# Performance work log

Hardware: AMD Instinct MI355X
Metric: run time of the kernel (lower is better)

The kernel has to match this reference:

```python
import jax, jax.numpy as jnp
import numpy as np

B, S, D, E = 8, 2048, 4096, 64
EXPERT_CAPACITY = 40  # seq_len / n_experts * 1.25


def setup_inputs() -> dict:
    key = jax.random.key(0)
    k1, k2 = jax.random.split(key)
    hidden_states = jax.random.normal(k1, (B, S, D), dtype=jnp.float32)
    W = jax.random.normal(k2, (D, E), dtype=jnp.float32) * (1.0 / np.sqrt(D))
    b = jnp.zeros((E,), dtype=jnp.float32)
    return {"hidden_states": hidden_states, "W": W, "b": b}


def reference(hidden_states, W, b):
    # router logits: [B, S, E] (jitter_noise == 0, router_dtype == float32)
    router_logits = jnp.einsum('bsd,de->bse', hidden_states, W) + b
    router_probs = jax.nn.softmax(router_logits, axis=-1)
    top1_probs = jnp.max(router_probs, axis=-1)                    # [B, S]
    expert_idx = jnp.argmax(router_probs, axis=-1)                 # [B, S]
    expert_indices = jax.nn.one_hot(expert_idx, E, dtype=jnp.int32)  # [B, S, E]
    # capacity masking: cumulative token priority per expert along seq dim
    token_priority = jnp.cumsum(expert_indices, axis=-2)           # [B, S, E]
    capacity_mask = token_priority <= EXPERT_CAPACITY
    expert_indices = expert_indices * capacity_mask.astype(jnp.int32)
    num_dropped = jnp.sum(jnp.sum(expert_indices, axis=-1) == 0)
    # aux load-balancing loss
    fi = jnp.sum(expert_indices, axis=-2).astype(router_probs.dtype) / S  # [B, E]
    pi = jnp.sum(router_probs, axis=-2) / S                               # [B, E]
    aux_loss = jnp.mean(E * jnp.sum(fi * pi, axis=-1))
    return (expert_indices, top1_probs, router_probs, aux_loss, num_dropped)
```

## Files before the change

### kernel.cpp

```cpp
#include <hip/hip_runtime.h>
#include <hip/hip_bf16.h>
#include <stdint.h>

#define Bb 8
#define Ss 2048
#define Dd 4096
#define Ee 64
#define CAP 40
#define M_TOK (Bb*Ss)
#define TOP1_OFF  (M_TOK*Ee)
#define PROBS_OFF (TOP1_OFF + M_TOK)
#define AUX_OFF   (PROBS_OFF + M_TOK*Ee)
#define ND_OFF    (AUX_OFF + 1)

#define W2_OFF   0u
#define PART_OFF (1u<<20)
#define CNTT_OFF (17u<<20)
#define PIT_OFF  ((17u<<20) + (64u<<10))
#define EID_OFF  ((17u<<20) + (128u<<10))

typedef __attribute__((ext_vector_type(8))) short short8;
typedef __attribute__((ext_vector_type(4))) float f32x4;

#define FENCE() do {                                                          \
    asm volatile("" ::: "memory");                                            \
    __builtin_amdgcn_sched_barrier(0);                                        \
  } while (0)

__device__ __forceinline__ void cvt8hl(const float4 a, const float4 b,
                                       short8& hi, short8& lo) {
  __hip_bfloat162 h0 = __float22bfloat162_rn(make_float2(a.x, a.y));
  __hip_bfloat162 h1 = __float22bfloat162_rn(make_float2(a.z, a.w));
  __hip_bfloat162 h2 = __float22bfloat162_rn(make_float2(b.x, b.y));
  __hip_bfloat162 h3 = __float22bfloat162_rn(make_float2(b.z, b.w));
  float2 f0 = __bfloat1622float2(h0), f1 = __bfloat1622float2(h1);
  float2 f2 = __bfloat1622float2(h2), f3 = __bfloat1622float2(h3);
  __hip_bfloat162 l0 = __float22bfloat162_rn(make_float2(a.x - f0.x, a.y - f0.y));
  __hip_bfloat162 l1 = __float22bfloat162_rn(make_float2(a.z - f1.x, a.w - f1.y));
  __hip_bfloat162 l2 = __float22bfloat162_rn(make_float2(b.x - f2.x, b.y - f2.y));
  __hip_bfloat162 l3 = __float22bfloat162_rn(make_float2(b.z - f3.x, b.w - f3.y));
  union U { __hip_bfloat162 h[4]; short8 s; };
  U uh; uh.h[0] = h0; uh.h[1] = h1; uh.h[2] = h2; uh.h[3] = h3; hi = uh.s;
  U ul; ul.h[0] = l0; ul.h[1] = l1; ul.h[2] = l2; ul.h[3] = l3; lo = ul.s;
}

__global__ __launch_bounds__(256) void k0_wsplit(const float* __restrict__ W,
                                                 char* __restrict__ w2) {
  const int id  = blockIdx.x * 256 + threadIdx.x;
  const int l   = id & 63;
  const int g   = (id >> 6) & 3;
  const int sub = (id >> 8) & 1;
  const int c   = id >> 9;
  const int e   = g * 16 + (l & 15);
  const int kb  = c * 64 + sub * 32 + (l >> 4) * 8;
  float xs[8];
#pragma unroll
  for (int j = 0; j < 8; ++j) xs[j] = W[(size_t)(kb + j) * Ee + e];
  short8 hi, lo;
  cvt8hl(make_float4(xs[0], xs[1], xs[2], xs[3]),
         make_float4(xs[4], xs[5], xs[6], xs[7]), hi, lo);
  char* base = w2 + (size_t)c * 16384 + sub * 8192 + g * 2048 + l * 16;
  *(short8*)base = hi;
  *(short8*)(base + 1024) = lo;
}

__global__ __launch_bounds__(256, 4) void k1_gemm(
    const float* __restrict__ H, const char* __restrict__ w2,
    float* __restrict__ part) {
  __shared__ char wb[4][8192];
  const int tid = threadIdx.x;
  const int wv = tid >> 6, l = tid & 63;
  const int tg = blockIdx.x >> 2, ks = blockIdx.x & 3;
  const float* hA = H + (size_t)(tg * 64 + wv * 16 + (l & 15)) * Dd
                      + ks * 1024 + (l >> 4) * 8;
  const char* wsrc = w2 + (size_t)ks * 262144 + wv * 2048 + l * 16;

  f32x4 acc[4];
#pragma unroll
  for (int g = 0; g < 4; ++g) acc[g] = (f32x4){0.f, 0.f, 0.f, 0.f};

  float4 aX0, aX1, aY0, aY1;
  short8 ah0, al0;

#define GLL16(gs, ls)                                                         \
  __builtin_amdgcn_global_load_lds(                                           \
      (const __attribute__((address_space(1))) unsigned int*)(gs),            \
      (__attribute__((address_space(3))) unsigned int*)(ls), 16, 0, 0)

#define STAGE(t, bi) {                                                        \
    const char* s_ = wsrc + (size_t)(t) * 8192;                               \
    char* d_ = &wb[bi][wv * 2048];                                            \
    GLL16(s_, d_); GLL16(s_ + 1024, d_ + 1024); }

#define LDA(r0, r1, t) { const float* p_ = hA + (t) * 32;                     \
    r0 = *(const float4*)(p_); r1 = *(const float4*)(p_ + 4); }

#define MFMA4(ac, ah, al, wh, wl) {                                           \
    ac = __builtin_amdgcn_mfma_f32_16x16x32_bf16(ah, wh, ac, 0, 0, 0);        \
    ac = __builtin_amdgcn_mfma_f32_16x16x32_bf16(ah, wl, ac, 0, 0, 0);        \
    ac = __builtin_amdgcn_mfma_f32_16x16x32_bf16(al, wh, ac, 0, 0, 0);        \
    ac = __builtin_amdgcn_mfma_f32_16x16x32_bf16(al, wl, ac, 0, 0, 0); }

#define COMPM(bi) { const char* wp_ = &wb[bi][0] + l * 16;                    \
    _Pragma("unroll")                                                         \
    for (int g = 0; g < 4; ++g) {                                             \
      const short8 wh = *(const short8*)(wp_ + g * 2048);                     \
      const short8 wl = *(const short8*)(wp_ + g * 2048 + 1024);              \
      MFMA4(acc[g], ah0, al0, wh, wl);                                        \
    } }

  STAGE(0, 0);
  FENCE();
  asm volatile("s_waitcnt vmcnt(0)" ::: "memory");
  __builtin_amdgcn_s_barrier();
  STAGE(1, 1);
  FENCE();
  LDA(aX0, aX1, 0);
  FENCE();
  STAGE(2, 2);
  FENCE();
  LDA(aY0, aY1, 1);
  FENCE();

#pragma unroll
  for (int t = 0; t < 32; ++t) {
    if (t < 30)       { asm volatile("s_waitcnt vmcnt(4)" ::: "memory"); }
    else if (t == 30) { asm volatile("s_waitcnt vmcnt(2)" ::: "memory"); }
    else              { asm volatile("s_waitcnt vmcnt(0)" ::: "memory"); }
    FENCE();
    if ((t & 1) == 0) { cvt8hl(aX0, aX1, ah0, al0); }
    else              { cvt8hl(aY0, aY1, ah0, al0); }
    FENCE();
    if (t <= 28) STAGE(t + 3, (t + 3) & 3);
    FENCE();
    if (t <= 29) {
      if ((t & 1) == 0) { LDA(aX0, aX1, t + 2); }
      else              { LDA(aY0, aY1, t + 2); }
    }
    FENCE();
    COMPM(t & 3);
    if (t < 31) __builtin_amdgcn_s_barrier();
  }

  float* pp = part + (size_t)(tg * 4 + ks) * 4096;
#pragma unroll
  for (int g = 0; g < 4; ++g)
#pragma unroll
    for (int r = 0; r < 4; ++r)
      pp[(wv * 16 + (l >> 4) * 4 + r) * 64 + g * 16 + (l & 15)] = acc[g][r];
}

__global__ __launch_bounds__(512) void k1b_softmax(
    const float* __restrict__ part, const float* __restrict__ bias,
    float* __restrict__ out, int* __restrict__ cntT, float* __restrict__ piT,
    int* __restrict__ eid_ws) {
  __shared__ int   csh[512];
  __shared__ float psh[512];
  const int tid = threadIdx.x, wv = tid >> 6, l = tid & 63;
  const int tg = blockIdx.x;
  const float* p0 = part + (size_t)tg * 16384;

  int cnt = 0; float pis = 0.f;
  const float bl_ = bias[l];
#pragma unroll
  for (int i = 0; i < 8; ++i) {
    const int t = wv * 8 + i, tok = tg * 64 + t;
    const float v = p0[t * 64 + l] + p0[4096 + t * 64 + l] +
                    p0[8192 + t * 64 + l] + p0[12288 + t * 64 + l] + bl_;
    float m = v; int mi = l;
#pragma unroll
    for (int off = 32; off >= 1; off >>= 1) {
      const float ov = __shfl_xor(m, off);
      const int   oi = __shfl_xor(mi, off);
      if (ov > m || (ov == m && oi < mi)) { m = ov; mi = oi; }
    }
    const float ex = __expf(v - m);
    float ssum = ex;
#pragma unroll
    for (int off = 32; off >= 1; off >>= 1) ssum += __shfl_xor(ssum, off);
    const float inv = 1.0f / ssum;
    const float p = ex * inv;
    out[(size_t)PROBS_OFF + (size_t)tok * Ee + l] = p;
    if (l == 0) {
      out[TOP1_OFF + tok] = inv;
      eid_ws[tok] = mi;
    }
    cnt += (mi == l) ? 1 : 0;
    pis += p;
  }
  csh[wv * 64 + l] = cnt;
  psh[wv * 64 + l] = pis;
  __syncthreads();
  if (tid < 64) {
    int ct = 0; float pp = 0.f;
#pragma unroll
    for (int w = 0; w < 8; ++w) { ct += csh[w * 64 + tid]; pp += psh[w * 64 + tid]; }
    cntT[((size_t)(tg >> 5) * 64 + tid) * 32 + (tg & 31)] = ct;
    piT [((size_t)(tg >> 5) * 64 + tid) * 32 + (tg & 31)] = pp;
  }
}

__global__ __launch_bounds__(64) void k3_indices(
    const int* __restrict__ cntT, const float* __restrict__ piT,
    const int* __restrict__ eid_ws, float* __restrict__ out) {
  __shared__ float tile[64][64];
  const int g = blockIdx.x, lane = threadIdx.x;
  const int b = g >> 5, cc = g & 31;
  const int tok = g * 64 + lane;
  const int e = eid_ws[tok];

  unsigned long long mymask = 0ull;
  for (int j = 0; j < 64; ++j) {
    const int ej = __shfl(e, j);
    const unsigned long long bal = __ballot(ej == e);
    if (j == lane) mymask = bal;
  }
  const int lrank = __popcll(mymask & ((1ull << lane) - 1ull));

  const int4* cp = (const int4*)(cntT + ((size_t)b * 64 + e) * 32);
  int prefix = 0;
#pragma unroll
  for (int j = 0; j < 8; ++j) {
    const int4 v = cp[j];
    const int base = 4 * j;
    prefix += ((base + 0 < cc) ? v.x : 0) + ((base + 1 < cc) ? v.y : 0)
            + ((base + 2 < cc) ? v.z : 0) + ((base + 3 < cc) ? v.w : 0);
  }
  const float keep = (prefix + lrank < CAP) ? 1.0f : 0.0f;

#pragma unroll
  for (int j = 0; j < 64; ++j) tile[j][lane] = 0.f;
  __syncthreads();
  tile[lane][e] = keep;
  __syncthreads();

  float4*       og = (float4*)(out + (size_t)g * 64 * 64);
  const float4* ts = (const float4*)&tile[0][0];
#pragma unroll
  for (int i = 0; i < 16; ++i) og[i * 64 + lane] = ts[i * 64 + lane];

  if (g == 0) {
    float auxsum = 0.f; int dropped = 0;
    for (int bb = 0; bb < 8; ++bb) {
      const int4*   cq = (const int4*)  (cntT + ((size_t)bb * 64 + lane) * 32);
      const float4* pq = (const float4*)(piT  + ((size_t)bb * 64 + lane) * 32);
      int tot = 0; float ps = 0.f;
#pragma unroll
      for (int j = 0; j < 8; ++j) {
        const int4 v = cq[j];   tot += v.x + v.y + v.z + v.w;
        const float4 w = pq[j]; ps  += w.x + w.y + w.z + w.w;
      }
      dropped += (tot > CAP) ? (tot - CAP) : 0;
      const float fi = (float)((tot < CAP) ? tot : CAP) * (1.0f / (float)Ss);
      const float pi = ps * (1.0f / (float)Ss);
      float fp = fi * pi;
#pragma unroll
      for (int off = 32; off >= 1; off >>= 1) fp += __shfl_xor(fp, off);
      auxsum += fp;
    }
#pragma unroll
    for (int off = 32; off >= 1; off >>= 1) dropped += __shfl_xor(dropped, off);
    if (lane == 0) {
      out[AUX_OFF] = (float)Ee * auxsum / (float)Bb;
      out[ND_OFF]  = (float)dropped;
    }
  }
}

extern "C" void kernel_launch(void* const* d_in, const int* in_sizes, int n_in,
                              void* d_out, int out_size, void* d_ws, size_t ws_size,
                              hipStream_t stream) {
  const float* H    = (const float*)d_in[0];
  const float* Wm   = (const float*)d_in[1];
  const float* bias = (const float*)d_in[2];
  float* out = (float*)d_out;
  char*  w2   = (char*) d_ws + W2_OFF;
  float* part = (float*)((char*)d_ws + PART_OFF);
  int*   cntT = (int*)  ((char*)d_ws + CNTT_OFF);
  float* piT  = (float*)((char*)d_ws + PIT_OFF);
  int*   eid  = (int*)  ((char*)d_ws + EID_OFF);

  hipLaunchKernelGGL(k0_wsplit,   dim3(128),  dim3(256), 0, stream, Wm, w2);
  hipLaunchKernelGGL(k1_gemm,     dim3(1024), dim3(256), 0, stream, H, w2, part);
  hipLaunchKernelGGL(k1b_softmax, dim3(256),  dim3(512), 0, stream,
                     part, bias, out, cntT, piT, eid);
  hipLaunchKernelGGL(k3_indices,  dim3(256),  dim3(64),  0, stream,
                     cntT, piT, eid, out);
}
```

Baseline: 90.24 us.

## Stage activation tiles through LDS via async global_load_lds with XOR swizzle

The GEMM kernel now loads the fp32 hidden-state tiles asynchronously into LDS with global_load_lds, alongside the weights, instead of holding them in register double-buffers. The LDS tiles use an XOR swizzle to avoid bank conflicts, and the bf16 hi/lo split now happens after reading from LDS. The barrier moves to the top of each iteration and the vmcnt thresholds are adjusted to match. LDS per block doubles and the launch-bounds occupancy hint drops from 4 to 2, so fewer blocks may be resident, in exchange for lower register pressure and fully asynchronous A loads.

```diff
diff --git a/kernel.cpp b/kernel.cpp
--- a/kernel.cpp
+++ b/kernel.cpp
@@ -64,22 +64,23 @@
   *(short8*)(base + 1024) = lo;
 }
 
-__global__ __launch_bounds__(256, 4) void k1_gemm(
+__global__ __launch_bounds__(256, 2) void k1_gemm(
     const float* __restrict__ H, const char* __restrict__ w2,
     float* __restrict__ part) {
-  __shared__ char wb[4][8192];
+  __shared__ char wb[4][16384];
   const int tid = threadIdx.x;
   const int wv = tid >> 6, l = tid & 63;
   const int tg = blockIdx.x >> 2, ks = blockIdx.x & 3;
-  const float* hA = H + (size_t)(tg * 64 + wv * 16 + (l & 15)) * Dd
-                      + ks * 1024 + (l >> 4) * 8;
+  const int tb = tg * 64;
   const char* wsrc = w2 + (size_t)ks * 262144 + wv * 2048 + l * 16;
+  const int swz = ((l & 7) ^ (l >> 3)) * 4;
+  const float* asrc0 = H + (size_t)(tb + wv * 8 + (l >> 3)) * Dd
+                         + ks * 1024 + swz;
+  const float* asrc1 = asrc0 + (size_t)32 * Dd;
 
   f32x4 acc[4];
 #pragma unroll
   for (int g = 0; g < 4; ++g) acc[g] = (f32x4){0.f, 0.f, 0.f, 0.f};
-
-  float4 aX0, aX1, aY0, aY1;
   short8 ah0, al0;
 
 #define GLL16(gs, ls)                                                         \
@@ -88,12 +89,14 @@
       (__attribute__((address_space(3))) unsigned int*)(ls), 16, 0, 0)
 
 #define STAGE(t, bi) {                                                        \
-    const char* s_ = wsrc + (size_t)(t) * 8192;                               \
-    char* d_ = &wb[bi][wv * 2048];                                            \
-    GLL16(s_, d_); GLL16(s_ + 1024, d_ + 1024); }
-
-#define LDA(r0, r1, t) { const float* p_ = hA + (t) * 32;                     \
-    r0 = *(const float4*)(p_); r1 = *(const float4*)(p_ + 4); }
+    const char* sw_ = wsrc + (size_t)(t) * 8192;                              \
+    char* dw_ = &wb[bi][wv * 2048];                                           \
+    GLL16(sw_, dw_); GLL16(sw_ + 1024, dw_ + 1024);                           \
+    const float* sa0_ = asrc0 + (t) * 32;                                     \
+    const float* sa1_ = asrc1 + (t) * 32;                                     \
+    char* da0_ = &wb[bi][8192 + wv * 1024];                                   \
+    char* da1_ = &wb[bi][8192 + 4096 + wv * 1024];                            \
+    GLL16(sa0_, da0_); GLL16(sa1_, da1_); }
 
 #define MFMA4(ac, ah, al, wh, wl) {                                           \
     ac = __builtin_amdgcn_mfma_f32_16x16x32_bf16(ah, wh, ac, 0, 0, 0);        \
@@ -101,7 +104,16 @@
     ac = __builtin_amdgcn_mfma_f32_16x16x32_bf16(al, wh, ac, 0, 0, 0);        \
     ac = __builtin_amdgcn_mfma_f32_16x16x32_bf16(al, wl, ac, 0, 0, 0); }
 
-#define COMPM(bi) { const char* wp_ = &wb[bi][0] + l * 16;                    \
+  const int arow = wv * 16 + (l & 15);
+  const int aslot0 = ((2 * (l >> 4))     ^ (arow & 7)) * 16;
+  const int aslot1 = ((2 * (l >> 4) + 1) ^ (arow & 7)) * 16;
+
+#define COMPM(bi) {                                                           \
+    const char* ab_ = &wb[bi][8192] + arow * 128;                             \
+    const float4 fa_ = *(const float4*)(ab_ + aslot0);                        \
+    const float4 fb_ = *(const float4*)(ab_ + aslot1);                        \
+    cvt8hl(fa_, fb_, ah0, al0);                                               \
+    const char* wp_ = &wb[bi][0] + l * 16;                                    \
     _Pragma("unroll")                                                         \
     for (int g = 0; g < 4; ++g) {                                             \
       const short8 wh = *(const short8*)(wp_ + g * 2048);                     \
@@ -111,35 +123,21 @@
 
   STAGE(0, 0);
   FENCE();
-  asm volatile("s_waitcnt vmcnt(0)" ::: "memory");
-  __builtin_amdgcn_s_barrier();
   STAGE(1, 1);
-  FENCE();
-  LDA(aX0, aX1, 0);
   FENCE();
   STAGE(2, 2);
   FENCE();
-  LDA(aY0, aY1, 1);
-  FENCE();
 
 #pragma unroll
   for (int t = 0; t < 32; ++t) {
-    if (t < 30)       { asm volatile("s_waitcnt vmcnt(4)" ::: "memory"); }
-    else if (t == 30) { asm volatile("s_waitcnt vmcnt(2)" ::: "memory"); }
+    if (t <= 29)      { asm volatile("s_waitcnt vmcnt(8)" ::: "memory"); }
+    else if (t == 30) { asm volatile("s_waitcnt vmcnt(4)" ::: "memory"); }
     else              { asm volatile("s_waitcnt vmcnt(0)" ::: "memory"); }
     FENCE();
-    if ((t & 1) == 0) { cvt8hl(aX0, aX1, ah0, al0); }
-    else              { cvt8hl(aY0, aY1, ah0, al0); }
-    FENCE();
+    __builtin_amdgcn_s_barrier();
     if (t <= 28) STAGE(t + 3, (t + 3) & 3);
     FENCE();
-    if (t <= 29) {
-      if ((t & 1) == 0) { LDA(aX0, aX1, t + 2); }
-      else              { LDA(aY0, aY1, t + 2); }
-    }
-    FENCE();
     COMPM(t & 3);
-    if (t < 31) __builtin_amdgcn_s_barrier();
   }
 
   float* pp = part + (size_t)(tg * 4 + ks) * 4096;
```

Measured after the change: 108.3 us. +20.1%, slower.
